# Optimization experiments

Measured on AMD Instinct MI355X. Metric: run time of the kernel, lower is better.

The kernel has to match this reference:

```python
import jax, jax.numpy as jnp
import numpy as np

B, S, D, H = 8, 512, 1024, 16
HD = D // H                      # head_dim = 64
MAX_SEQ_LEN = 512
SCRATCH_SLOTS = 64


def _rope_cache():
    inv_freq = 1.0 / (10000.0 ** (jnp.arange(0, HD, 2, dtype=jnp.float32) / HD))
    t = jnp.arange(MAX_SEQ_LEN + SCRATCH_SLOTS, dtype=jnp.float32)
    freqs = jnp.outer(t, inv_freq)               # [T, HD//2]
    freqs = jnp.concatenate([freqs, freqs], -1)  # [T, HD]
    return jnp.sin(freqs), jnp.cos(freqs)


def rotate_half(x):
    x1, x2 = x[..., : x.shape[-1] // 2], x[..., x.shape[-1] // 2 :]
    return jnp.concatenate([-x2, x1], axis=-1)


def setup_inputs() -> dict:
    key = jax.random.key(0)
    ks = jax.random.split(key, 5)
    def w(k):
        return jax.random.normal(k, (D, D), dtype=jnp.float32) * 0.02
    return {
        "x": jax.random.normal(ks[0], (B, S, D), dtype=jnp.float32),
        "Wq": w(ks[1]), "bq": jnp.zeros((D,), jnp.float32),
        "Wk": w(ks[2]), "bk": jnp.zeros((D,), jnp.float32),
        "Wv": w(ks[3]), "bv": jnp.zeros((D,), jnp.float32),
        "Wo": w(ks[4]), "bo": jnp.zeros((D,), jnp.float32),
    }


def reference(x, Wq, bq, Wk, bk, Wv, bv, Wo, bo):
    b, s, d = x.shape
    sin_c, cos_c = _rope_cache()
    scale = jnp.array(HD ** (-0.5), dtype=jnp.float32)

    xh = x.astype(jnp.float16)
    def lin(inp, W, bias):  # nnx.Linear with dtype=fp16: cast params + input to fp16
        return inp @ W.astype(jnp.float16) + bias.astype(jnp.float16)

    q = lin(xh, Wq, bq).reshape(b, s, H, HD)
    k = lin(xh, Wk, bk).reshape(b, s, H, HD)
    v = lin(xh, Wv, bv).reshape(b, s, H, HD)

    sin = sin_c[:s, None, :].astype(jnp.float32)  # [s,1,HD]
    cos = cos_c[:s, None, :].astype(jnp.float32)
    qf = q.astype(jnp.float32)
    kf = k.astype(jnp.float32)
    q = qf * cos + rotate_half(qf) * sin
    k = kf * cos + rotate_half(kf) * sin
    v = v.astype(jnp.float32)
    q = q * scale  # module's explicit scale

    # [b,H,s,HD]
    q, k, v = (t.transpose(0, 2, 1, 3) for t in (q, k, v))

    # jax.nn.dot_product_attention additionally scales by 1/sqrt(HD)
    logits = jnp.einsum("bhqd,bhkd->bhqk", q, k) * scale
    probs = jax.nn.softmax(logits, axis=-1)
    out = jnp.einsum("bhqk,bhkd->bhqd", probs, v)
    out = out.transpose(0, 2, 1, 3).reshape(b, s, d)
    return lin(out.astype(jnp.float16), Wo, bo)
```

## Files before the change

kernel.cpp:

```cpp
#include <hip/hip_runtime.h>

typedef _Float16 half8 __attribute__((ext_vector_type(8)));
typedef _Float16 half4v __attribute__((ext_vector_type(4)));
typedef float f32x4 __attribute__((ext_vector_type(4)));

#define OFF_CS    0u
#define OFF_XH    (1u<<20)
#define OFF_WQKVT (OFF_XH + 8u*1024u*1024u)
#define OFF_WOT   (OFF_WQKVT + 8u*1024u*1024u)
#define OFF_QKV   (OFF_WOT + 2u*1024u*1024u)
#define OFF_ATTN  OFF_WQKVT


__device__ __forceinline__ void gload16(const _Float16* g, _Float16* l) {
  __builtin_amdgcn_global_load_lds((const __attribute__((address_space(1))) void*)g,
                                   (__attribute__((address_space(3))) void*)l, 16, 0, 0);
}

__global__ void prep_k(const float* __restrict__ x,
                       const float* __restrict__ W0, const float* __restrict__ W1,
                       const float* __restrict__ W2, const float* __restrict__ W3,
                       _Float16* __restrict__ xh, _Float16* __restrict__ wqkvt,
                       _Float16* __restrict__ wot, float2* __restrict__ cs) {
  int bid = blockIdx.x, tid = threadIdx.x;
  if (bid < 4096) {
    int i = bid * 256 + tid;
    float4 v = ((const float4*)x)[i];
    half4v h;
    h[0] = (_Float16)v.x; h[1] = (_Float16)v.y; h[2] = (_Float16)v.z; h[3] = (_Float16)v.w;
    *(half4v*)(xh + (size_t)i * 4) = h;
  } else if (bid < 8192) {
    __shared__ float tile[32][33];
    int tb = bid - 4096;
    int z = tb >> 10, t = tb & 1023, by = t >> 5, bx = t & 31;
    const float* W = z == 0 ? W0 : z == 1 ? W1 : z == 2 ? W2 : W3;
    _Float16* Wt = z < 3 ? wqkvt + (size_t)z * 1048576 : wot;
    int r = tid >> 3, c0 = (tid & 7) * 4;
    float4 v = *(const float4*)(W + (size_t)(by * 32 + r) * 1024 + bx * 32 + c0);
    tile[r][c0] = v.x; tile[r][c0 + 1] = v.y; tile[r][c0 + 2] = v.z; tile[r][c0 + 3] = v.w;
    __syncthreads();
    half4v h;
#pragma unroll
    for (int j = 0; j < 4; j++) h[j] = (_Float16)tile[c0 + j][r];
    *(half4v*)(Wt + (size_t)(bx * 32 + r) * 1024 + by * 32 + c0) = h;
  } else {
    int idx = (bid - 8192) * 256 + tid;
    int pos = idx >> 5, j = idx & 31;
    float inv = powf(10000.0f, -(float)j * (1.0f / 32.0f));
    float f = (float)pos * inv;
    cs[idx] = make_float2(cosf(f), sinf(f));
  }
}

template <int MODE>
__global__ __launch_bounds__(256, MODE == 0 ? 3 : 2) void gemm_k(
    const _Float16* __restrict__ A, const _Float16* __restrict__ Bt,
    const float* __restrict__ b0, const float* __restrict__ b1, const float* __restrict__ b2,
    void* __restrict__ Cv, const float2* __restrict__ cs) {
  constexpr int BM  = (MODE == 0) ? 128 : 64;
  constexpr int N   = (MODE == 0) ? 3072 : 1024;
  constexpr int NBX = N / 128;
  constexpr int MF  = BM / 32;
  constexpr int ACH = BM / 64;
  __shared__ _Float16 Ar[3][BM * 32];
  __shared__ _Float16 Br[3][128 * 32];

  int nwg = gridDim.x, cpx = nwg >> 3;
  int bid = blockIdx.x;
  int wgid = (bid & 7) * cpx + (bid >> 3);
  int by = wgid / NBX, bx = wgid % NBX;

  int tid = threadIdx.x, lane = tid & 63, w = tid >> 6;
  int wr = w >> 1, wc = w & 1;
  int arow = lane & 15, ag = lane >> 4;
  int s8 = (((arow & 1) << 2) | ag) ^ ((arow >> 1) & 7);

  int qq = (lane & 7) ^ (lane >> 3);
  int rloc = ((lane >> 3) << 1) + (qq >> 2);
  int gcol = (qq & 3) * 8;

  const _Float16* Ag = A + (size_t)(by * BM) * 1024;
  const _Float16* Bg = Bt + (size_t)(bx * 128) * 1024;

  f32x4 acc[MF][4] = {};

  auto stage = [&](int t) {
    int slot = t % 3;
    int k0 = t * 32;
#pragma unroll
    for (int i = 0; i < ACH; i++) {
      int c = w * ACH + i;
      gload16(Ag + (size_t)(c * 16 + rloc) * 1024 + k0 + gcol, &Ar[slot][c * 512]);
    }
#pragma unroll
    for (int i = 0; i < 2; i++) {
      int c = w * 2 + i;
      gload16(Bg + (size_t)(c * 16 + rloc) * 1024 + k0 + gcol, &Br[slot][c * 512]);
    }
  };

  stage(0); stage(1);
  if (MODE == 0) asm volatile("s_waitcnt vmcnt(4)" ::: "memory");
  else           asm volatile("s_waitcnt vmcnt(3)" ::: "memory");
  __builtin_amdgcn_s_barrier();
  __builtin_amdgcn_sched_barrier(0);

  for (int t = 0; t < 32; ++t) {
    if (t < 30) stage(t + 2);
    __builtin_amdgcn_sched_barrier(0);
    const _Float16* Ac = &Ar[t % 3][0];
    const _Float16* Bc = &Br[t % 3][0];
    half8 a[MF], b[4];
#pragma unroll
    for (int m = 0; m < MF; m++) {
      int R = wr * (BM / 2) + m * 16 + arow;
      a[m] = *(const half8*)&Ac[(R >> 1) * 64 + s8 * 8];
    }
#pragma unroll
    for (int n = 0; n < 4; n++) {
      int R = wc * 64 + n * 16 + arow;
      b[n] = *(const half8*)&Bc[(R >> 1) * 64 + s8 * 8];
    }
    __builtin_amdgcn_s_setprio(1);
#pragma unroll
    for (int m = 0; m < MF; m++)
#pragma unroll
      for (int n = 0; n < 4; n++)
        acc[m][n] = __builtin_amdgcn_mfma_f32_16x16x32_f16(a[m], b[n], acc[m][n], 0, 0, 0);
    __builtin_amdgcn_s_setprio(0);
    __builtin_amdgcn_sched_barrier(0);
    if (t < 30) {
      if (MODE == 0) asm volatile("s_waitcnt vmcnt(4)" ::: "memory");
      else           asm volatile("s_waitcnt vmcnt(3)" ::: "memory");
    } else if (t == 30) {
      asm volatile("s_waitcnt vmcnt(0)" ::: "memory");
    }
    if (t < 31) {
      __builtin_amdgcn_s_barrier();
      __builtin_amdgcn_sched_barrier(0);
    }
  }

  int gc0 = bx * 128 + wc * 64;
  if (MODE == 0) {
    const float* bp = gc0 < 1024 ? b0 : (gc0 < 2048 ? b1 : b2);
    float bb_[4];
#pragma unroll
    for (int n = 0; n < 4; n++) bb_[n] = bp[(gc0 & 1023) + n * 16 + arow];
    _Float16* C = (_Float16*)Cv;
    if (gc0 < 2048) {
      bool isQ = gc0 < 1024;
#pragma unroll
      for (int m = 0; m < MF; m++) {
        int gr = by * BM + wr * (BM / 2) + m * 16 + ag * 4;
#pragma unroll
        for (int r = 0; r < 4; r++) {
          int row = gr + r, pos = row & 511;
#pragma unroll
          for (int n = 0; n < 2; n++) {
            int j = n * 16 + arow;
            float av = (float)(_Float16)(acc[m][n][r] + bb_[n]);
            float bv = (float)(_Float16)(acc[m][n + 2][r] + bb_[n + 2]);
            float2 tt = cs[pos * 32 + j];
            float o0 = av * tt.x - bv * tt.y;
            float o1 = bv * tt.x + av * tt.y;
            if (isQ) { o0 *= 0.015625f; o1 *= 0.015625f; }
            C[(size_t)row * 3072 + gc0 + j]      = (_Float16)o0;
            C[(size_t)row * 3072 + gc0 + j + 32] = (_Float16)o1;
          }
        }
      }
    } else {
#pragma unroll
      for (int m = 0; m < MF; m++) {
        int gr = by * BM + wr * (BM / 2) + m * 16 + ag * 4;
        int bb2 = gr >> 9;
        int st6 = (gr & 511) >> 6;
        int s63 = gr & 63;
#pragma unroll
        for (int n = 0; n < 4; n++) {
          int colh = gc0 - 2048 + n * 16 + arow;
          int h = colh >> 6, hd = colh & 63;
          half4v v4;
#pragma unroll
          for (int r = 0; r < 4; r++) v4[r] = (_Float16)(acc[m][n][r] + bb_[n]);
          size_t addr = ((size_t)(bb2 * 512 + hd * 8 + st6)) * 3072 + 2048 + h * 64 + s63;
          *(half4v*)(C + addr) = v4;
        }
      }
    }
  } else {
    float* C = (float*)Cv;
#pragma unroll
    for (int m = 0; m < MF; m++) {
      int gr = by * BM + wr * (BM / 2) + m * 16 + ag * 4;
#pragma unroll
      for (int n = 0; n < 4; n++) {
        int gc = gc0 + n * 16 + arow;
        float bb = b0[gc];
#pragma unroll
        for (int r = 0; r < 4; r++)
          C[(size_t)(gr + r) * 1024 + gc] = (float)(_Float16)(acc[m][n][r] + bb);
      }
    }
  }
}

__global__ __launch_bounds__(256, 2) void attn_k(const _Float16* __restrict__ qkv,
                                                 _Float16* __restrict__ out) {
  int id = blockIdx.x;
  int bh = id & 127, qt = id >> 7;
  int b = bh >> 4, h = bh & 15;
  int tid = threadIdx.x, lane = tid & 63, w = tid >> 6;
  int arow = lane & 15, ag = lane >> 4;

  __shared__ _Float16 Ks[64 * 64];
  __shared__ _Float16 Vs[64 * 64];
  __shared__ _Float16 Pl[4][32][72];

  int qrow0 = b * 512 + qt * 128 + w * 32;
  const _Float16* Qp = qkv + (size_t)qrow0 * 3072 + h * 64;
  half8 qa[2][2];
#pragma unroll
  for (int g = 0; g < 2; g++)
#pragma unroll
    for (int ks = 0; ks < 2; ks++)
      qa[g][ks] = *(const half8*)(Qp + (size_t)(g * 16 + arow) * 3072 + ks * 32 + ag * 8);

  const _Float16* Kb = qkv + (size_t)(b * 512) * 3072 + 1024 + h * 64;

  int srow = lane >> 3;
  int sslot = (lane & 7) ^ srow;
  const _Float16* Ksrc0 = Kb + (size_t)(w * 16 + srow) * 3072 + sslot * 8;
  const _Float16* Vsrc0 = qkv + ((size_t)(b * 512) + (w * 16 + srow) * 8) * 3072
                          + 2048 + h * 64 + sslot * 8;

  int rs = arow & 7;

  float psl[2][4] = {};
  f32x4 oacc[2][4] = {};

  for (int st = 0; st < 8; ++st) {
#pragma unroll
    for (int i = 0; i < 2; i++) {
      gload16(Ksrc0 + (size_t)(st * 64 + i * 8) * 3072, &Ks[(w * 16 + i * 8) * 64]);
      gload16(Vsrc0 + (size_t)(i * 64 + st) * 3072,     &Vs[(w * 16 + i * 8) * 64]);
    }
    __syncthreads();

    f32x4 lg[2][4];
#pragma unroll
    for (int c = 0; c < 4; c++) {
      f32x4 a0 = {}, a1 = {};
#pragma unroll
      for (int ks = 0; ks < 2; ks++) {
        int slot = (ks * 4 + ag) ^ rs;
        half8 kb = *(const half8*)&Ks[(c * 16 + arow) * 64 + slot * 8];
        a0 = __builtin_amdgcn_mfma_f32_16x16x32_f16(qa[0][ks], kb, a0, 0, 0, 0);
        a1 = __builtin_amdgcn_mfma_f32_16x16x32_f16(qa[1][ks], kb, a1, 0, 0, 0);
      }
      lg[0][c] = a0;
      lg[1][c] = a1;
    }
#pragma unroll
    for (int g = 0; g < 2; g++) {
      _Float16 ph[4][4];
#pragma unroll
      for (int r = 0; r < 4; r++)
#pragma unroll
        for (int c = 0; c < 4; c++) {
          float p = __builtin_amdgcn_exp2f(lg[g][c][r] * 1.44269504f);
          psl[g][r] += p;
          ph[c][r] = (_Float16)p;
        }
#pragma unroll
      for (int c = 0; c < 4; c++)
#pragma unroll
        for (int r = 0; r < 4; r++)
          Pl[w][g * 16 + ag * 4 + r][c * 16 + arow] = ph[c][r];
    }
#pragma unroll
    for (int ks = 0; ks < 2; ks++) {
      half8 pa0 = *(const half8*)&Pl[w][arow][ks * 32 + ag * 8];
      half8 pa1 = *(const half8*)&Pl[w][16 + arow][ks * 32 + ag * 8];
#pragma unroll
      for (int c = 0; c < 4; c++) {
        int slot = (ks * 4 + ag) ^ rs;
        half8 vb = *(const half8*)&Vs[(c * 16 + arow) * 64 + slot * 8];
        oacc[0][c] = __builtin_amdgcn_mfma_f32_16x16x32_f16(pa0, vb, oacc[0][c], 0, 0, 0);
        oacc[1][c] = __builtin_amdgcn_mfma_f32_16x16x32_f16(pa1, vb, oacc[1][c], 0, 0, 0);
      }
    }
    __syncthreads();
  }
#pragma unroll
  for (int g = 0; g < 2; g++)
#pragma unroll
    for (int r = 0; r < 4; r++)
#pragma unroll
      for (int d = 1; d < 16; d <<= 1) psl[g][r] += __shfl_xor(psl[g][r], d, 16);
#pragma unroll
  for (int g = 0; g < 2; g++)
#pragma unroll
    for (int c = 0; c < 4; c++)
#pragma unroll
      for (int r = 0; r < 4; r++) {
        float v = oacc[g][c][r] / psl[g][r];
        out[(size_t)(qrow0 + g * 16 + ag * 4 + r) * 1024 + h * 64 + c * 16 + arow] =
            (_Float16)v;
      }
}

extern "C" void kernel_launch(void* const* d_in, const int* in_sizes, int n_in,
                              void* d_out, int out_size, void* d_ws, size_t ws_size,
                              hipStream_t stream) {
  const float* x  = (const float*)d_in[0];
  const float* Wq = (const float*)d_in[1];
  const float* bq = (const float*)d_in[2];
  const float* Wk = (const float*)d_in[3];
  const float* bk = (const float*)d_in[4];
  const float* Wv = (const float*)d_in[5];
  const float* bv = (const float*)d_in[6];
  const float* Wo = (const float*)d_in[7];
  const float* bo = (const float*)d_in[8];

  char* ws = (char*)d_ws;
  float2* cs      = (float2*)(ws + OFF_CS);
  _Float16* xh    = (_Float16*)(ws + OFF_XH);
  _Float16* wqkvt = (_Float16*)(ws + OFF_WQKVT);
  _Float16* wot   = (_Float16*)(ws + OFF_WOT);
  _Float16* qkv   = (_Float16*)(ws + OFF_QKV);
  _Float16* attn  = (_Float16*)(ws + OFF_ATTN);

  prep_k<<<8256, 256, 0, stream>>>(x, Wq, Wk, Wv, Wo, xh, wqkvt, wot, cs);
  gemm_k<0><<<768, 256, 0, stream>>>(xh, wqkvt, bq, bk, bv, qkv, cs);
  attn_k<<<512, 256, 0, stream>>>(qkv, attn);
  gemm_k<1><<<512, 256, 0, stream>>>(attn, wot, bo, bo, bo, d_out, cs);
}
```

Baseline: 89.34 us.

## Give each wave private LDS tiles in QKV GEMM to drop block barriers

The QKV projection GEMM now gives each of the four waves its own double-buffered LDS region. Each wave loads its own 64-row A slice and 64-column B slice and waits only on its own vmcnt, so the per-iteration workgroup barrier is gone. In exchange, each wave now loads its A and B slices separately instead of sharing them across the block, which increases global-to-LDS traffic. LDS use also rises to 64 KB and occupancy drops from 3 to 2 blocks. The output GEMM is split into its own non-templated kernel with the same logic as before.

```diff
diff --git a/kernel.cpp b/kernel.cpp
--- a/kernel.cpp
+++ b/kernel.cpp
@@ -52,23 +52,15 @@
   }
 }
 
-template <int MODE>
-__global__ __launch_bounds__(256, MODE == 0 ? 3 : 2) void gemm_k(
+__global__ __launch_bounds__(256, 2) void gemm_qkv_k(
     const _Float16* __restrict__ A, const _Float16* __restrict__ Bt,
     const float* __restrict__ b0, const float* __restrict__ b1, const float* __restrict__ b2,
-    void* __restrict__ Cv, const float2* __restrict__ cs) {
-  constexpr int BM  = (MODE == 0) ? 128 : 64;
-  constexpr int N   = (MODE == 0) ? 3072 : 1024;
-  constexpr int NBX = N / 128;
-  constexpr int MF  = BM / 32;
-  constexpr int ACH = BM / 64;
-  __shared__ _Float16 Ar[3][BM * 32];
-  __shared__ _Float16 Br[3][128 * 32];
-
-  int nwg = gridDim.x, cpx = nwg >> 3;
+    _Float16* __restrict__ C, const float2* __restrict__ cs) {
+  __shared__ _Float16 L[4][2][4096];
+
   int bid = blockIdx.x;
-  int wgid = (bid & 7) * cpx + (bid >> 3);
-  int by = wgid / NBX, bx = wgid % NBX;
+  int wgid = (bid & 7) * 96 + (bid >> 3);
+  int by = wgid / 24, bx = wgid % 24;
 
   int tid = threadIdx.x, lane = tid & 63, w = tid >> 6;
   int wr = w >> 1, wc = w & 1;
@@ -79,19 +71,130 @@
   int rloc = ((lane >> 3) << 1) + (qq >> 2);
   int gcol = (qq & 3) * 8;
 
+  const _Float16* Ag = A + (size_t)(by * 128 + wr * 64) * 1024;
+  const _Float16* Bg = Bt + (size_t)(bx * 128 + wc * 64) * 1024;
+
+  f32x4 acc[4][4] = {};
+
+  auto stage = [&](int t) {
+    _Float16* dst = &L[w][t & 1][0];
+    int k0 = t * 32;
+#pragma unroll
+    for (int i = 0; i < 4; i++)
+      gload16(Ag + (size_t)(i * 16 + rloc) * 1024 + k0 + gcol, dst + i * 512);
+#pragma unroll
+    for (int i = 0; i < 4; i++)
+      gload16(Bg + (size_t)(i * 16 + rloc) * 1024 + k0 + gcol, dst + 2048 + i * 512);
+  };
+
+  stage(0);
+
+  for (int t = 0; t < 32; ++t) {
+    if (t < 31) stage(t + 1);
+    __builtin_amdgcn_sched_barrier(0);
+    if (t < 31) asm volatile("s_waitcnt vmcnt(8)" ::: "memory");
+    else        asm volatile("s_waitcnt vmcnt(0)" ::: "memory");
+    __builtin_amdgcn_sched_barrier(0);
+    const _Float16* Lc = &L[w][t & 1][0];
+    half8 a[4], b[4];
+#pragma unroll
+    for (int m = 0; m < 4; m++) {
+      int R = m * 16 + arow;
+      a[m] = *(const half8*)&Lc[(R >> 1) * 64 + s8 * 8];
+    }
+#pragma unroll
+    for (int n = 0; n < 4; n++) {
+      int R = n * 16 + arow;
+      b[n] = *(const half8*)&Lc[2048 + (R >> 1) * 64 + s8 * 8];
+    }
+    __builtin_amdgcn_s_setprio(1);
+#pragma unroll
+    for (int m = 0; m < 4; m++)
+#pragma unroll
+      for (int n = 0; n < 4; n++)
+        acc[m][n] = __builtin_amdgcn_mfma_f32_16x16x32_f16(a[m], b[n], acc[m][n], 0, 0, 0);
+    __builtin_amdgcn_s_setprio(0);
+  }
+
+  int gc0 = bx * 128 + wc * 64;
+  const float* bp = gc0 < 1024 ? b0 : (gc0 < 2048 ? b1 : b2);
+  float bb_[4];
+#pragma unroll
+  for (int n = 0; n < 4; n++) bb_[n] = bp[(gc0 & 1023) + n * 16 + arow];
+
+  if (gc0 < 2048) {
+    bool isQ = gc0 < 1024;
+#pragma unroll
+    for (int m = 0; m < 4; m++) {
+      int gr = by * 128 + wr * 64 + m * 16 + ag * 4;
+#pragma unroll
+      for (int r = 0; r < 4; r++) {
+        int row = gr + r, pos = row & 511;
+#pragma unroll
+        for (int n = 0; n < 2; n++) {
+          int j = n * 16 + arow;
+          float av = (float)(_Float16)(acc[m][n][r] + bb_[n]);
+          float bv = (float)(_Float16)(acc[m][n + 2][r] + bb_[n + 2]);
+          float2 tt = cs[pos * 32 + j];
+          float o0 = av * tt.x - bv * tt.y;
+          float o1 = bv * tt.x + av * tt.y;
+          if (isQ) { o0 *= 0.015625f; o1 *= 0.015625f; }
+          C[(size_t)row * 3072 + gc0 + j]      = (_Float16)o0;
+          C[(size_t)row * 3072 + gc0 + j + 32] = (_Float16)o1;
+        }
+      }
+    }
+  } else {
+#pragma unroll
+    for (int m = 0; m < 4; m++) {
+      int gr = by * 128 + wr * 64 + m * 16 + ag * 4;
+      int bb2 = gr >> 9;
+      int st6 = (gr & 511) >> 6;
+      int s63 = gr & 63;
+#pragma unroll
+      for (int n = 0; n < 4; n++) {
+        int colh = gc0 - 2048 + n * 16 + arow;
+        int h = colh >> 6, hd = colh & 63;
+        half4v v4;
+#pragma unroll
+        for (int r = 0; r < 4; r++) v4[r] = (_Float16)(acc[m][n][r] + bb_[n]);
+        size_t addr = ((size_t)(bb2 * 512 + hd * 8 + st6)) * 3072 + 2048 + h * 64 + s63;
+        *(half4v*)(C + addr) = v4;
+      }
+    }
+  }
+}
+
+__global__ __launch_bounds__(256, 2) void gemm_out_k(
+    const _Float16* __restrict__ A, const _Float16* __restrict__ Bt,
+    const float* __restrict__ b0, float* __restrict__ Cv) {
+  constexpr int BM = 64;
+  __shared__ _Float16 Ar[3][BM * 32];
+  __shared__ _Float16 Br[3][128 * 32];
+
+  int nwg = gridDim.x, cpx = nwg >> 3;
+  int bid = blockIdx.x;
+  int wgid = (bid & 7) * cpx + (bid >> 3);
+  int by = wgid / 8, bx = wgid % 8;
+
+  int tid = threadIdx.x, lane = tid & 63, w = tid >> 6;
+  int wr = w >> 1, wc = w & 1;
+  int arow = lane & 15, ag = lane >> 4;
+  int s8 = (((arow & 1) << 2) | ag) ^ ((arow >> 1) & 7);
+
+  int qq = (lane & 7) ^ (lane >> 3);
+  int rloc = ((lane >> 3) << 1) + (qq >> 2);
+  int gcol = (qq & 3) * 8;
+
   const _Float16* Ag = A + (size_t)(by * BM) * 1024;
   const _Float16* Bg = Bt + (size_t)(bx * 128) * 1024;
 
-  f32x4 acc[MF][4] = {};
+  f32x4 acc[2][4] = {};
 
   auto stage = [&](int t) {
     int slot = t % 3;
     int k0 = t * 32;
-#pragma unroll
-    for (int i = 0; i < ACH; i++) {
-      int c = w * ACH + i;
-      gload16(Ag + (size_t)(c * 16 + rloc) * 1024 + k0 + gcol, &Ar[slot][c * 512]);
-    }
+    gload16(Ag + (size_t)(w * 16 + rloc) * 1024 + k0 + gcol, &Ar[slot][w * 512]);
 #pragma unroll
     for (int i = 0; i < 2; i++) {
       int c = w * 2 + i;
@@ -100,8 +203,7 @@
   };
 
   stage(0); stage(1);
-  if (MODE == 0) asm volatile("s_waitcnt vmcnt(4)" ::: "memory");
-  else           asm volatile("s_waitcnt vmcnt(3)" ::: "memory");
+  asm volatile("s_waitcnt vmcnt(3)" ::: "memory");
   __builtin_amdgcn_s_barrier();
   __builtin_amdgcn_sched_barrier(0);
 
@@ -110,10 +212,10 @@
     __builtin_amdgcn_sched_barrier(0);
     const _Float16* Ac = &Ar[t % 3][0];
     const _Float16* Bc = &Br[t % 3][0];
-    half8 a[MF], b[4];
-#pragma unroll
-    for (int m = 0; m < MF; m++) {
-      int R = wr * (BM / 2) + m * 16 + arow;
+    half8 a[2], b[4];
+#pragma unroll
+    for (int m = 0; m < 2; m++) {
+      int R = wr * 32 + m * 16 + arow;
       a[m] = *(const half8*)&Ac[(R >> 1) * 64 + s8 * 8];
     }
 #pragma unroll
@@ -123,85 +225,30 @@
     }
     __builtin_amdgcn_s_setprio(1);
 #pragma unroll
-    for (int m = 0; m < MF; m++)
+    for (int m = 0; m < 2; m++)
 #pragma unroll
       for (int n = 0; n < 4; n++)
         acc[m][n] = __builtin_amdgcn_mfma_f32_16x16x32_f16(a[m], b[n], acc[m][n], 0, 0, 0);
     __builtin_amdgcn_s_setprio(0);
     __builtin_amdgcn_sched_barrier(0);
-    if (t < 30) {
-      if (MODE == 0) asm volatile("s_waitcnt vmcnt(4)" ::: "memory");
-      else           asm volatile("s_waitcnt vmcnt(3)" ::: "memory");
-    } else if (t == 30) {
-      asm volatile("s_waitcnt vmcnt(0)" ::: "memory");
-    }
+    if (t < 30)       asm volatile("s_waitcnt vmcnt(3)" ::: "memory");
+    else if (t == 30) asm volatile("s_waitcnt vmcnt(0)" ::: "memory");
     if (t < 31) {
       __builtin_amdgcn_s_barrier();
       __builtin_amdgcn_sched_barrier(0);
     }
   }
 
-  int gc0 = bx * 128 + wc * 64;
-  if (MODE == 0) {
-    const float* bp = gc0 < 1024 ? b0 : (gc0 < 2048 ? b1 : b2);
-    float bb_[4];
-#pragma unroll
-    for (int n = 0; n < 4; n++) bb_[n] = bp[(gc0 & 1023) + n * 16 + arow];
-    _Float16* C = (_Float16*)Cv;
-    if (gc0 < 2048) {
-      bool isQ = gc0 < 1024;
-#pragma unroll
-      for (int m = 0; m < MF; m++) {
-        int gr = by * BM + wr * (BM / 2) + m * 16 + ag * 4;
-#pragma unroll
-        for (int r = 0; r < 4; r++) {
-          int row = gr + r, pos = row & 511;
-#pragma unroll
-          for (int n = 0; n < 2; n++) {
-            int j = n * 16 + arow;
-            float av = (float)(_Float16)(acc[m][n][r] + bb_[n]);
-            float bv = (float)(_Float16)(acc[m][n + 2][r] + bb_[n + 2]);
-            float2 tt = cs[pos * 32 + j];
-            float o0 = av * tt.x - bv * tt.y;
-            float o1 = bv * tt.x + av * tt.y;
-            if (isQ) { o0 *= 0.015625f; o1 *= 0.015625f; }
-            C[(size_t)row * 3072 + gc0 + j]      = (_Float16)o0;
-            C[(size_t)row * 3072 + gc0 + j + 32] = (_Float16)o1;
-          }
-        }
-      }
-    } else {
-#pragma unroll
-      for (int m = 0; m < MF; m++) {
-        int gr = by * BM + wr * (BM / 2) + m * 16 + ag * 4;
-        int bb2 = gr >> 9;
-        int st6 = (gr & 511) >> 6;
-        int s63 = gr & 63;
-#pragma unroll
-        for (int n = 0; n < 4; n++) {
-          int colh = gc0 - 2048 + n * 16 + arow;
-          int h = colh >> 6, hd = colh & 63;
-          half4v v4;
-#pragma unroll
-          for (int r = 0; r < 4; r++) v4[r] = (_Float16)(acc[m][n][r] + bb_[n]);
-          size_t addr = ((size_t)(bb2 * 512 + hd * 8 + st6)) * 3072 + 2048 + h * 64 + s63;
-          *(half4v*)(C + addr) = v4;
-        }
-      }
-    }
-  } else {
-    float* C = (float*)Cv;
-#pragma unroll
-    for (int m = 0; m < MF; m++) {
-      int gr = by * BM + wr * (BM / 2) + m * 16 + ag * 4;
-#pragma unroll
-      for (int n = 0; n < 4; n++) {
-        int gc = gc0 + n * 16 + arow;
-        float bb = b0[gc];
-#pragma unroll
-        for (int r = 0; r < 4; r++)
-          C[(size_t)(gr + r) * 1024 + gc] = (float)(_Float16)(acc[m][n][r] + bb);
-      }
+#pragma unroll
+  for (int m = 0; m < 2; m++) {
+    int gr = by * BM + wr * 32 + m * 16 + ag * 4;
+#pragma unroll
+    for (int n = 0; n < 4; n++) {
+      int gc = bx * 128 + wc * 64 + n * 16 + arow;
+      float bb = b0[gc];
+#pragma unroll
+      for (int r = 0; r < 4; r++)
+        Cv[(size_t)(gr + r) * 1024 + gc] = (float)(_Float16)(acc[m][n][r] + bb);
     }
   }
 }
@@ -333,7 +380,7 @@
   _Float16* attn  = (_Float16*)(ws + OFF_ATTN);
 
   prep_k<<<8256, 256, 0, stream>>>(x, Wq, Wk, Wv, Wo, xh, wqkvt, wot, cs);
-  gemm_k<0><<<768, 256, 0, stream>>>(xh, wqkvt, bq, bk, bv, qkv, cs);
+  gemm_qkv_k<<<768, 256, 0, stream>>>(xh, wqkvt, bq, bk, bv, qkv, cs);
   attn_k<<<512, 256, 0, stream>>>(qkv, attn);
-  gemm_k<1><<<512, 256, 0, stream>>>(attn, wot, bo, bo, bo, d_out, cs);
-}
+  gemm_out_k<<<512, 256, 0, stream>>>(attn, wot, bo, (float*)d_out);
+}
```

Measured after the change: 99.85 us. 1.12x slower.
